# Kernel tuning notes

Measured on AMD Instinct MI355X. Metric: run time of the kernel, lower is better.

The kernel has to match this reference:

```python
import jax, jax.numpy as jnp
import numpy as np

N_NODES = 50000
N_EDGES = 600000
N_LABEL = 200000
IN_CH = 128
OUT_CH = 128
K_HOPS = 2


def setup_inputs() -> dict:
    key = jax.random.key(0)
    ks = jax.random.split(key, 9)
    x = jax.random.normal(ks[0], (N_NODES, IN_CH), dtype=jnp.float32)
    edge_index = jax.random.randint(ks[1], (2, N_EDGES), 0, N_NODES)
    edge_label_index = jax.random.randint(ks[2], (2, N_LABEL), 0, N_NODES)
    conv_weight = jax.random.normal(ks[3], (OUT_CH, IN_CH), dtype=jnp.float32) * 0.05
    conv_bias = jax.random.normal(ks[4], (OUT_CH,), dtype=jnp.float32) * 0.05
    w1 = jax.random.normal(ks[5], (OUT_CH // 2, OUT_CH), dtype=jnp.float32) * 0.05
    b1 = jax.random.normal(ks[6], (OUT_CH // 2,), dtype=jnp.float32) * 0.05
    w2 = jax.random.normal(ks[7], (1, OUT_CH // 2), dtype=jnp.float32) * 0.05
    b2 = jax.random.normal(ks[8], (1,), dtype=jnp.float32) * 0.05
    return {"x": x, "edge_index": edge_index, "edge_label_index": edge_label_index,
            "conv_weight": conv_weight, "conv_bias": conv_bias,
            "w1": w1, "b1": b1, "w2": w2, "b2": b2}


def reference(x, edge_index, edge_label_index, conv_weight, conv_bias, w1, b1, w2, b2):
    n = x.shape[0]
    # gcn_norm with self-loops: A_hat = D^{-1/2} (A + I) D^{-1/2}
    loop = jnp.arange(n, dtype=edge_index.dtype)
    src = jnp.concatenate([edge_index[0], loop])  # message sources
    dst = jnp.concatenate([edge_index[1], loop])  # aggregation targets
    deg = jax.ops.segment_sum(jnp.ones_like(dst, dtype=x.dtype), dst, num_segments=n)
    dinv = jnp.where(deg > 0, jax.lax.rsqrt(deg), 0.0)
    w = dinv[src] * dinv[dst]  # [E+N] edge weights

    # K-hop propagation: h <- A_hat h, repeated K times (SGConv)
    h = x
    for _ in range(K_HOPS):
        h = jax.ops.segment_sum(h[src] * w[:, None], dst, num_segments=n)
    z = h @ conv_weight.T + conv_bias  # [N, out_channels]

    # decode: gather endpoint embeddings, multiply, tiny MLP (dropout inactive at eval)
    s = z[edge_label_index[0]] * z[edge_label_index[1]]  # [E_label, out]
    h1 = jax.nn.relu(s @ w1.T + b1)
    r = (h1 @ w2.T + b2).sum(axis=-1)  # [E_label]
    return r
```

## Files before the change

### kernel.cpp

```cpp
#include <hip/hip_runtime.h>

#define N_CH 128

typedef _Float16 half8  __attribute__((ext_vector_type(8)));
typedef _Float16 half4v __attribute__((ext_vector_type(4)));
typedef float    floatx4 __attribute__((ext_vector_type(4)));


__global__ void k_zero(int* __restrict__ cnt, int n) {
    int i = blockIdx.x * blockDim.x + threadIdx.x;
    if (i < n) cnt[i] = 0;
}

__global__ void k_count(const int* __restrict__ dst, int* __restrict__ cnt, int E) {
    int e = blockIdx.x * blockDim.x + threadIdx.x;
    if (e < E) atomicAdd(&cnt[dst[e]], 1);
}

__global__ __launch_bounds__(1024) void k_scan1(const int* __restrict__ cnt,
                                                int* __restrict__ offs,
                                                int* __restrict__ bsum, int n) {
    __shared__ int ssum[16];
    int tid = threadIdx.x;
    int lane = tid & 63, wid = tid >> 6;
    int i = blockIdx.x * 1024 + tid;
    int v = (i < n) ? cnt[i] : 0;
    int x = v;
    #pragma unroll
    for (int off = 1; off < 64; off <<= 1) {
        int y = __shfl_up(x, off, 64);
        if (lane >= off) x += y;
    }
    if (lane == 63) ssum[wid] = x;
    __syncthreads();
    if (wid == 0 && lane < 16) {
        int s = ssum[lane];
        #pragma unroll
        for (int off = 1; off < 16; off <<= 1) {
            int y = __shfl_up(s, off, 64);
            if (lane >= off) s += y;
        }
        ssum[lane] = s;
    }
    __syncthreads();
    int waveoff = (wid > 0) ? ssum[wid - 1] : 0;
    int incl = x + waveoff;
    if (i < n) offs[i] = incl - v;
    if (tid == 1023) bsum[blockIdx.x] = incl;
}

__global__ __launch_bounds__(64) void k_scan2(const int* __restrict__ bsum,
                                              int* __restrict__ bbase, int nb) {
    int lane = threadIdx.x;
    int v = (lane < nb) ? bsum[lane] : 0;
    int x = v;
    #pragma unroll
    for (int off = 1; off < 64; off <<= 1) {
        int y = __shfl_up(x, off, 64);
        if (lane >= off) x += y;
    }
    if (lane < nb) bbase[lane] = x - v;
}

__global__ void k_scan3(const int* __restrict__ cnt, int* __restrict__ offs,
                        const int* __restrict__ bbase, int* __restrict__ cur,
                        float* __restrict__ dinv, int n) {
    int i = blockIdx.x * blockDim.x + threadIdx.x;
    if (i < n) {
        int o = offs[i] + bbase[i >> 10];
        offs[i] = o;
        cur[i]  = o;
        dinv[i] = rsqrtf((float)(cnt[i] + 1));
    }
}

__global__ void k_fill(const int* __restrict__ src, const int* __restrict__ dst,
                       int* __restrict__ cur, int* __restrict__ csr, int E) {
    int e = blockIdx.x * blockDim.x + threadIdx.x;
    if (e < E) {
        int p = atomicAdd(&cur[dst[e]], 1);
        csr[p] = src[e];
    }
}


__global__ void k_cvt(const float* __restrict__ x, const float* __restrict__ dinv,
                      _Float16* __restrict__ u0, _Float16* __restrict__ u1,
                      const float* __restrict__ W,  _Float16* __restrict__ wh,
                      const float* __restrict__ W1, _Float16* __restrict__ w1h,
                      int n) {
    int nx4  = n * (N_CH / 4);
    int nw4  = N_CH * N_CH / 4;
    int nw14 = 64 * N_CH / 4;
    int i = blockIdx.x * blockDim.x + threadIdx.x;
    if (i < nx4) {
        float d = dinv[i >> 5];
        float4 v = ((const float4*)x)[i];
        half4v o;
        o[0] = (_Float16)(d * v.x); o[1] = (_Float16)(d * v.y);
        o[2] = (_Float16)(d * v.z); o[3] = (_Float16)(d * v.w);
        ((half4v*)u0)[i] = o;
        return;
    }
    int j = i - nx4;
    if (j < nw4) {
        float4 v = ((const float4*)W)[j];
        half4v o;
        o[0] = (_Float16)v.x; o[1] = (_Float16)v.y; o[2] = (_Float16)v.z; o[3] = (_Float16)v.w;
        ((half4v*)wh)[j] = o;
        return;
    }
    j -= nw4;
    if (j < nw14) {
        float4 v = ((const float4*)W1)[j];
        half4v o;
        o[0] = (_Float16)v.x; o[1] = (_Float16)v.y; o[2] = (_Float16)v.z; o[3] = (_Float16)v.w;
        ((half4v*)w1h)[j] = o;
        return;
    }
    j -= nw14;
    if (j < 64) {
        half4v zz; zz[0] = (_Float16)0.f; zz[1] = (_Float16)0.f; zz[2] = (_Float16)0.f; zz[3] = (_Float16)0.f;
        _Float16* dst16 = (j < 32) ? u0 : u1;
        ((half4v*)(dst16 + (size_t)n * N_CH))[j & 31] = zz;
    }
}


__global__ __launch_bounds__(256) void k_hop16(const _Float16* __restrict__ hin,
                                               _Float16* __restrict__ hout,
                                               const int* __restrict__ offs,
                                               const int* __restrict__ cnt,
                                               const float* __restrict__ dinv,
                                               const int* __restrict__ csr,
                                               int n, int squared) {
    int tid  = threadIdx.x;
    int node = blockIdx.x * 16 + (tid >> 4);
    int c16  = tid & 15;
    if (node >= n) return;
    float di = dinv[node];
    float sc = squared ? di * di : di;
    int s0 = offs[node], c = cnt[node];
    const int* lst = csr + s0;
    half8 self = ((const half8*)(hin + (size_t)node * N_CH))[c16];
    float acc[8];
    #pragma unroll
    for (int j = 0; j < 8; ++j) acc[j] = (float)self[j];
    for (int t0 = 0; t0 < c; t0 += 8) {
        int idx[8];
        #pragma unroll
        for (int i = 0; i < 8; ++i) {
            int t = t0 + i;
            int v = lst[t];
            idx[i] = (t < c) ? v : n;
        }
        half8 u[8];
        #pragma unroll
        for (int i = 0; i < 8; ++i)
            u[i] = ((const half8*)(hin + (size_t)idx[i] * N_CH))[c16];
        #pragma unroll
        for (int i = 0; i < 8; ++i)
            #pragma unroll
            for (int j = 0; j < 8; ++j) acc[j] += (float)u[i][j];
    }
    half8 o;
    #pragma unroll
    for (int j = 0; j < 8; ++j) o[j] = (_Float16)(sc * acc[j]);
    ((half8*)(hout + (size_t)node * N_CH))[c16] = o;
}


__global__ __launch_bounds__(256) void k_zlin_mfma(const _Float16* __restrict__ h,
                                                   const _Float16* __restrict__ wh,
                                                   const float* __restrict__ bc,
                                                   _Float16* __restrict__ z, int n) {
    __shared__ half8 wls[128 * 16];
    int tid = threadIdx.x;
    int lane = tid & 63, w = tid >> 6;
    int quad = lane >> 4, m16 = lane & 15;
    int nb = blockIdx.x * 64;
    #pragma unroll
    for (int i = 0; i < 8; ++i) {
        int g = tid + 256 * i;
        int r = g >> 4, c = g & 15;
        wls[r * 16 + (c ^ (r & 15))] = ((const half8*)wh)[g];
    }
    int arow = nb + w * 16 + m16;
    const half8* hrow = (const half8*)(h + (size_t)arow * N_CH);
    half8 a[4];
    #pragma unroll
    for (int kk = 0; kk < 4; ++kk) a[kk] = hrow[kk * 4 + quad];
    __syncthreads();
    int outnode0 = nb + w * 16 + quad * 4;
    #pragma unroll
    for (int jt = 0; jt < 8; ++jt) {
        floatx4 acc = {0.f, 0.f, 0.f, 0.f};
        #pragma unroll
        for (int kk = 0; kk < 4; ++kk) {
            int r = jt * 16 + m16;
            half8 bfr = wls[r * 16 + ((kk * 4 + quad) ^ m16)];
            acc = __builtin_amdgcn_mfma_f32_16x16x32_f16(a[kk], bfr, acc, 0, 0, 0);
        }
        int j = jt * 16 + m16;
        float bias = bc[j];
        #pragma unroll
        for (int reg = 0; reg < 4; ++reg) {
            int node = outnode0 + reg;
            if (node < n) z[(size_t)node * N_CH + j] = (_Float16)(acc[reg] + bias);
        }
    }
}


__global__ __launch_bounds__(256) void k_decode_mfma(const _Float16* __restrict__ z,
        const int* __restrict__ ai, const int* __restrict__ bi,
        const _Float16* __restrict__ w1h, const float* __restrict__ b1,
        const float* __restrict__ w2, const float* __restrict__ b2,
        float* __restrict__ out, int m) {
    __shared__ half8 w1ls[64 * 16];
    __shared__ half8 sls[64 * 16];
    int tid = threadIdx.x;
    int lane = tid & 63, w = tid >> 6;
    int quad = lane >> 4, m16 = lane & 15;
    int pbase = blockIdx.x * 64;
    #pragma unroll
    for (int i = 0; i < 4; ++i) {
        int g = tid + 256 * i;
        int r = g >> 4, c = g & 15;
        w1ls[r * 16 + (c ^ (r & 15))] = ((const half8*)w1h)[g];
    }
    int pidx = pbase + w * 16 + m16;
    if (pidx >= m) pidx = m - 1;
    int idxa = ai[pidx];
    int idxb = bi[pidx];
    #pragma unroll
    for (int it = 0; it < 4; ++it) {
        int p = it * 4 + quad;
        int ia = __shfl(idxa, p, 64);
        int ib = __shfl(idxb, p, 64);
        half8 za = ((const half8*)(z + (size_t)ia * N_CH))[m16];
        half8 zb = ((const half8*)(z + (size_t)ib * N_CH))[m16];
        half8 s8 = za * zb;
        int pp = w * 16 + p;
        sls[pp * 16 + (m16 ^ (pp & 15))] = s8;
    }
    __syncthreads();
    half8 a[4];
    #pragma unroll
    for (int kk = 0; kk < 4; ++kk)
        a[kk] = sls[(w * 16 + m16) * 16 + ((kk * 4 + quad) ^ m16)];
    float rsum[4] = {0.f, 0.f, 0.f, 0.f};
    #pragma unroll
    for (int jt = 0; jt < 4; ++jt) {
        floatx4 acc = {0.f, 0.f, 0.f, 0.f};
        #pragma unroll
        for (int kk = 0; kk < 4; ++kk) {
            int r = jt * 16 + m16;
            half8 bfr = w1ls[r * 16 + ((kk * 4 + quad) ^ m16)];
            acc = __builtin_amdgcn_mfma_f32_16x16x32_f16(a[kk], bfr, acc, 0, 0, 0);
        }
        int j = jt * 16 + m16;
        float b1j = b1[j], w2j = w2[j];
        #pragma unroll
        for (int reg = 0; reg < 4; ++reg) {
            float v = fmaxf(acc[reg] + b1j, 0.f) * w2j;
            v += __shfl_xor(v, 1, 64);
            v += __shfl_xor(v, 2, 64);
            v += __shfl_xor(v, 4, 64);
            v += __shfl_xor(v, 8, 64);
            rsum[reg] += v;
        }
    }
    if (m16 == 0) {
        float bb = b2[0];
        #pragma unroll
        for (int reg = 0; reg < 4; ++reg) {
            int gp = pbase + w * 16 + quad * 4 + reg;
            if (gp < m) out[gp] = rsum[reg] + bb;
        }
    }
}


extern "C" void kernel_launch(void* const* d_in, const int* in_sizes, int n_in,
                              void* d_out, int out_size, void* d_ws, size_t ws_size,
                              hipStream_t stream) {
    const float* x   = (const float*)d_in[0];
    const int*   ei  = (const int*)d_in[1];
    const int*   eli = (const int*)d_in[2];
    const float* W   = (const float*)d_in[3];
    const float* bc  = (const float*)d_in[4];
    const float* W1  = (const float*)d_in[5];
    const float* b1  = (const float*)d_in[6];
    const float* w2  = (const float*)d_in[7];
    const float* b2  = (const float*)d_in[8];
    float* out = (float*)d_out;

    const int N = in_sizes[0] / N_CH;
    const int E = in_sizes[1] / 2;
    const int M = in_sizes[2] / 2;

    const int* src = ei;
    const int* dst = ei + E;
    const int* ai  = eli;
    const int* bi  = eli + M;

    _Float16* hb0 = (_Float16*)d_ws;
    _Float16* hb1 = hb0 + (size_t)(N + 1) * N_CH;
    _Float16* wh  = hb1 + (size_t)(N + 1) * N_CH;
    _Float16* w1h = wh + 16384;
    int*   csr  = (int*)(w1h + 8192);
    int*   cnt  = csr + E;
    int*   off  = cnt + N;
    int*   cur  = off + N;
    float* dnv  = (float*)(cur + N);
    int*   bsum = (int*)(dnv + N);
    int*   bbas = bsum + 64;

    int nb = (N + 1023) / 1024;
    k_zero<<<(N + 255) / 256, 256, 0, stream>>>(cnt, N);
    k_count<<<(E + 255) / 256, 256, 0, stream>>>(dst, cnt, E);
    k_scan1<<<nb, 1024, 0, stream>>>(cnt, off, bsum, N);
    k_scan2<<<1, 64, 0, stream>>>(bsum, bbas, nb);
    k_scan3<<<(N + 255) / 256, 256, 0, stream>>>(cnt, off, bbas, cur, dnv, N);
    k_fill<<<(E + 255) / 256, 256, 0, stream>>>(src, dst, cur, csr, E);
    int tot4 = N * (N_CH / 4) + N_CH * N_CH / 4 + 64 * N_CH / 4 + 64;
    k_cvt<<<(tot4 + 255) / 256, 256, 0, stream>>>(x, dnv, hb0, hb1, W, wh, W1, w1h, N);

    int hop_blocks = (N + 15) / 16;
    k_hop16<<<hop_blocks, 256, 0, stream>>>(hb0, hb1, off, cnt, dnv, csr, N, 1);
    k_hop16<<<hop_blocks, 256, 0, stream>>>(hb1, hb0, off, cnt, dnv, csr, N, 0);

    k_zlin_mfma<<<(N + 63) / 64, 256, 0, stream>>>(hb0, wh, bc, hb1, N);

    k_decode_mfma<<<(M + 63) / 64, 256, 0, stream>>>(hb1, ai, bi, w1h, b1, w2, b2, out, M);
}
```

Measured before the change: 233.7 us.

## Widen hop gather batch, use fdot2 accumulation, batch decode loads, memset counts

The hop kernel now gathers 16 neighbor rows per batch instead of 8, which puts more independent loads in flight. It accumulates each half pair into fp32 with fdot2 instead of separate converts and adds. The decode kernel issues all endpoint gathers before multiplying, so the loads can overlap. The zeroing kernel is replaced by hipMemsetAsync. The cost is higher register pressure in the hop kernel and wasted padded loads for low-degree nodes, which is most of them at an average degree of about 12.

Result: slower. 239.1 us (+2.3%).

```diff
diff --git a/kernel.cpp b/kernel.cpp
--- a/kernel.cpp
+++ b/kernel.cpp
@@ -4,13 +4,9 @@
 
 typedef _Float16 half8  __attribute__((ext_vector_type(8)));
 typedef _Float16 half4v __attribute__((ext_vector_type(4)));
+typedef _Float16 half2v __attribute__((ext_vector_type(2)));
 typedef float    floatx4 __attribute__((ext_vector_type(4)));
 
-
-__global__ void k_zero(int* __restrict__ cnt, int n) {
-    int i = blockIdx.x * blockDim.x + threadIdx.x;
-    if (i < n) cnt[i] = 0;
-}
 
 __global__ void k_count(const int* __restrict__ dst, int* __restrict__ cnt, int E) {
     int e = blockIdx.x * blockDim.x + threadIdx.x;
@@ -143,25 +139,34 @@
     int s0 = offs[node], c = cnt[node];
     const int* lst = csr + s0;
     half8 self = ((const half8*)(hin + (size_t)node * N_CH))[c16];
+    const half2v c10 = {(_Float16)1.0f, (_Float16)0.0f};
+    const half2v c01 = {(_Float16)0.0f, (_Float16)1.0f};
     float acc[8];
     #pragma unroll
     for (int j = 0; j < 8; ++j) acc[j] = (float)self[j];
-    for (int t0 = 0; t0 < c; t0 += 8) {
-        int idx[8];
-        #pragma unroll
-        for (int i = 0; i < 8; ++i) {
+    for (int t0 = 0; t0 < c; t0 += 16) {
+        int idx[16];
+        #pragma unroll
+        for (int i = 0; i < 16; ++i) {
             int t = t0 + i;
             int v = lst[t];
             idx[i] = (t < c) ? v : n;
         }
-        half8 u[8];
-        #pragma unroll
-        for (int i = 0; i < 8; ++i)
+        half8 u[16];
+        #pragma unroll
+        for (int i = 0; i < 16; ++i)
             u[i] = ((const half8*)(hin + (size_t)idx[i] * N_CH))[c16];
         #pragma unroll
-        for (int i = 0; i < 8; ++i)
+        for (int i = 0; i < 16; ++i) {
             #pragma unroll
-            for (int j = 0; j < 8; ++j) acc[j] += (float)u[i][j];
+            for (int p = 0; p < 4; ++p) {
+                half2v pair;
+                pair[0] = u[i][2 * p];
+                pair[1] = u[i][2 * p + 1];
+                acc[2 * p]     = __builtin_amdgcn_fdot2(pair, c10, acc[2 * p], false);
+                acc[2 * p + 1] = __builtin_amdgcn_fdot2(pair, c01, acc[2 * p + 1], false);
+            }
+        }
     }
     half8 o;
     #pragma unroll
@@ -233,15 +238,23 @@
     if (pidx >= m) pidx = m - 1;
     int idxa = ai[pidx];
     int idxb = bi[pidx];
+    int ia[4], ib[4];
     #pragma unroll
     for (int it = 0; it < 4; ++it) {
         int p = it * 4 + quad;
-        int ia = __shfl(idxa, p, 64);
-        int ib = __shfl(idxb, p, 64);
-        half8 za = ((const half8*)(z + (size_t)ia * N_CH))[m16];
-        half8 zb = ((const half8*)(z + (size_t)ib * N_CH))[m16];
-        half8 s8 = za * zb;
-        int pp = w * 16 + p;
+        ia[it] = __shfl(idxa, p, 64);
+        ib[it] = __shfl(idxb, p, 64);
+    }
+    half8 za[4], zb[4];
+    #pragma unroll
+    for (int it = 0; it < 4; ++it) {
+        za[it] = ((const half8*)(z + (size_t)ia[it] * N_CH))[m16];
+        zb[it] = ((const half8*)(z + (size_t)ib[it] * N_CH))[m16];
+    }
+    #pragma unroll
+    for (int it = 0; it < 4; ++it) {
+        half8 s8 = za[it] * zb[it];
+        int pp = w * 16 + it * 4 + quad;
         sls[pp * 16 + (m16 ^ (pp & 15))] = s8;
     }
     __syncthreads();
@@ -318,7 +331,7 @@
     int*   bbas = bsum + 64;
 
     int nb = (N + 1023) / 1024;
-    k_zero<<<(N + 255) / 256, 256, 0, stream>>>(cnt, N);
+    (void)hipMemsetAsync(cnt, 0, (size_t)N * sizeof(int), stream);
     k_count<<<(E + 255) / 256, 256, 0, stream>>>(dst, cnt, E);
     k_scan1<<<nb, 1024, 0, stream>>>(cnt, off, bsum, N);
     k_scan2<<<1, 64, 0, stream>>>(bsum, bbas, nb);
```

## Merge setup kernels, single-block scan, 16-bit CSR indices, batched decode gathers

Applied to the files above, without the earlier changes.

Folds the zeroing kernel and the weight conversion into one prep kernel and replaces the three-kernel scan with a single-block looping scan, which cuts kernel launches. CSR neighbor indices are stored as 16-bit unsigned values to halve index traffic in the hop kernels. The decode kernel now issues all endpoint gathers before using any of them, to raise memory-level parallelism. The single-block scan serialises about 50 iterations on one CU. The 16-bit indices only cover node ids below 65536, which holds for this input size.

Measured after the change: 278.2 us. 1.19x slower.

```diff
diff --git a/kernel.cpp b/kernel.cpp
--- a/kernel.cpp
+++ b/kernel.cpp
@@ -7,92 +7,94 @@
 typedef float    floatx4 __attribute__((ext_vector_type(4)));
 
 
-__global__ void k_zero(int* __restrict__ cnt, int n) {
+__global__ void k_prep(const float* __restrict__ x, const float* __restrict__ dinv_unused,
+                       int* __restrict__ cnt,
+                       const float* __restrict__ W,  _Float16* __restrict__ wh,
+                       const float* __restrict__ W1, _Float16* __restrict__ w1h,
+                       int n) {
     int i = blockIdx.x * blockDim.x + threadIdx.x;
     if (i < n) cnt[i] = 0;
-}
+    int nw4  = N_CH * N_CH / 4;
+    int nw14 = 64 * N_CH / 4;
+    if (i < nw4) {
+        float4 v = ((const float4*)W)[i];
+        half4v o;
+        o[0] = (_Float16)v.x; o[1] = (_Float16)v.y; o[2] = (_Float16)v.z; o[3] = (_Float16)v.w;
+        ((half4v*)wh)[i] = o;
+    } else if (i < nw4 + nw14) {
+        int j = i - nw4;
+        float4 v = ((const float4*)W1)[j];
+        half4v o;
+        o[0] = (_Float16)v.x; o[1] = (_Float16)v.y; o[2] = (_Float16)v.z; o[3] = (_Float16)v.w;
+        ((half4v*)w1h)[j] = o;
+    }
+}
+
 
 __global__ void k_count(const int* __restrict__ dst, int* __restrict__ cnt, int E) {
     int e = blockIdx.x * blockDim.x + threadIdx.x;
     if (e < E) atomicAdd(&cnt[dst[e]], 1);
 }
 
-__global__ __launch_bounds__(1024) void k_scan1(const int* __restrict__ cnt,
-                                                int* __restrict__ offs,
-                                                int* __restrict__ bsum, int n) {
+__global__ __launch_bounds__(1024) void k_scan(const int* __restrict__ cnt,
+                                               int* __restrict__ offs,
+                                               int* __restrict__ cur,
+                                               float* __restrict__ dinv, int n) {
     __shared__ int ssum[16];
+    __shared__ int sbase;
     int tid = threadIdx.x;
     int lane = tid & 63, wid = tid >> 6;
-    int i = blockIdx.x * 1024 + tid;
-    int v = (i < n) ? cnt[i] : 0;
-    int x = v;
-    #pragma unroll
-    for (int off = 1; off < 64; off <<= 1) {
-        int y = __shfl_up(x, off, 64);
-        if (lane >= off) x += y;
-    }
-    if (lane == 63) ssum[wid] = x;
+    if (tid == 0) sbase = 0;
     __syncthreads();
-    if (wid == 0 && lane < 16) {
-        int s = ssum[lane];
-        #pragma unroll
-        for (int off = 1; off < 16; off <<= 1) {
-            int y = __shfl_up(s, off, 64);
-            if (lane >= off) s += y;
-        }
-        ssum[lane] = s;
-    }
-    __syncthreads();
-    int waveoff = (wid > 0) ? ssum[wid - 1] : 0;
-    int incl = x + waveoff;
-    if (i < n) offs[i] = incl - v;
-    if (tid == 1023) bsum[blockIdx.x] = incl;
-}
-
-__global__ __launch_bounds__(64) void k_scan2(const int* __restrict__ bsum,
-                                              int* __restrict__ bbase, int nb) {
-    int lane = threadIdx.x;
-    int v = (lane < nb) ? bsum[lane] : 0;
-    int x = v;
-    #pragma unroll
-    for (int off = 1; off < 64; off <<= 1) {
-        int y = __shfl_up(x, off, 64);
-        if (lane >= off) x += y;
-    }
-    if (lane < nb) bbase[lane] = x - v;
-}
-
-__global__ void k_scan3(const int* __restrict__ cnt, int* __restrict__ offs,
-                        const int* __restrict__ bbase, int* __restrict__ cur,
-                        float* __restrict__ dinv, int n) {
-    int i = blockIdx.x * blockDim.x + threadIdx.x;
-    if (i < n) {
-        int o = offs[i] + bbase[i >> 10];
-        offs[i] = o;
-        cur[i]  = o;
-        dinv[i] = rsqrtf((float)(cnt[i] + 1));
+    for (int base = 0; base < n; base += 1024) {
+        int i = base + tid;
+        int v = (i < n) ? cnt[i] : 0;
+        int x = v;
+        #pragma unroll
+        for (int off = 1; off < 64; off <<= 1) {
+            int y = __shfl_up(x, off, 64);
+            if (lane >= off) x += y;
+        }
+        if (lane == 63) ssum[wid] = x;
+        __syncthreads();
+        if (wid == 0 && lane < 16) {
+            int s = ssum[lane];
+            #pragma unroll
+            for (int off = 1; off < 16; off <<= 1) {
+                int y = __shfl_up(s, off, 64);
+                if (lane >= off) s += y;
+            }
+            ssum[lane] = s;
+        }
+        __syncthreads();
+        int waveoff = (wid > 0) ? ssum[wid - 1] : 0;
+        int incl = x + waveoff + sbase;
+        if (i < n) {
+            int excl = incl - v;
+            offs[i] = excl;
+            cur[i]  = excl;
+            dinv[i] = rsqrtf((float)(v + 1));
+        }
+        __syncthreads();
+        if (tid == 1023) sbase = incl;
+        __syncthreads();
     }
 }
 
 __global__ void k_fill(const int* __restrict__ src, const int* __restrict__ dst,
-                       int* __restrict__ cur, int* __restrict__ csr, int E) {
+                       int* __restrict__ cur, unsigned short* __restrict__ csr, int E) {
     int e = blockIdx.x * blockDim.x + threadIdx.x;
     if (e < E) {
         int p = atomicAdd(&cur[dst[e]], 1);
-        csr[p] = src[e];
-    }
-}
-
-
-__global__ void k_cvt(const float* __restrict__ x, const float* __restrict__ dinv,
-                      _Float16* __restrict__ u0, _Float16* __restrict__ u1,
-                      const float* __restrict__ W,  _Float16* __restrict__ wh,
-                      const float* __restrict__ W1, _Float16* __restrict__ w1h,
-                      int n) {
-    int nx4  = n * (N_CH / 4);
-    int nw4  = N_CH * N_CH / 4;
-    int nw14 = 64 * N_CH / 4;
+        csr[p] = (unsigned short)src[e];
+    }
+}
+
+
+__global__ void k_scale(const float* __restrict__ x, const float* __restrict__ dinv,
+                        _Float16* __restrict__ u0, _Float16* __restrict__ u1, int n) {
     int i = blockIdx.x * blockDim.x + threadIdx.x;
+    int nx4 = n * (N_CH / 4);
     if (i < nx4) {
         float d = dinv[i >> 5];
         float4 v = ((const float4*)x)[i];
@@ -100,26 +102,8 @@
         o[0] = (_Float16)(d * v.x); o[1] = (_Float16)(d * v.y);
         o[2] = (_Float16)(d * v.z); o[3] = (_Float16)(d * v.w);
         ((half4v*)u0)[i] = o;
-        return;
-    }
-    int j = i - nx4;
-    if (j < nw4) {
-        float4 v = ((const float4*)W)[j];
-        half4v o;
-        o[0] = (_Float16)v.x; o[1] = (_Float16)v.y; o[2] = (_Float16)v.z; o[3] = (_Float16)v.w;
-        ((half4v*)wh)[j] = o;
-        return;
-    }
-    j -= nw4;
-    if (j < nw14) {
-        float4 v = ((const float4*)W1)[j];
-        half4v o;
-        o[0] = (_Float16)v.x; o[1] = (_Float16)v.y; o[2] = (_Float16)v.z; o[3] = (_Float16)v.w;
-        ((half4v*)w1h)[j] = o;
-        return;
-    }
-    j -= nw14;
-    if (j < 64) {
+    } else if (i < nx4 + 64) {
+        int j = i - nx4;
         half4v zz; zz[0] = (_Float16)0.f; zz[1] = (_Float16)0.f; zz[2] = (_Float16)0.f; zz[3] = (_Float16)0.f;
         _Float16* dst16 = (j < 32) ? u0 : u1;
         ((half4v*)(dst16 + (size_t)n * N_CH))[j & 31] = zz;
@@ -132,7 +116,7 @@
                                                const int* __restrict__ offs,
                                                const int* __restrict__ cnt,
                                                const float* __restrict__ dinv,
-                                               const int* __restrict__ csr,
+                                               const unsigned short* __restrict__ csr,
                                                int n, int squared) {
     int tid  = threadIdx.x;
     int node = blockIdx.x * 16 + (tid >> 4);
@@ -141,7 +125,7 @@
     float di = dinv[node];
     float sc = squared ? di * di : di;
     int s0 = offs[node], c = cnt[node];
-    const int* lst = csr + s0;
+    const unsigned short* lst = csr + s0;
     half8 self = ((const half8*)(hin + (size_t)node * N_CH))[c16];
     float acc[8];
     #pragma unroll
@@ -151,8 +135,8 @@
         #pragma unroll
         for (int i = 0; i < 8; ++i) {
             int t = t0 + i;
-            int v = lst[t];
-            idx[i] = (t < c) ? v : n;
+            unsigned short v = lst[t];
+            idx[i] = (t < c) ? (int)v : n;
         }
         half8 u[8];
         #pragma unroll
@@ -233,15 +217,23 @@
     if (pidx >= m) pidx = m - 1;
     int idxa = ai[pidx];
     int idxb = bi[pidx];
+    int ia[4], ib[4];
     #pragma unroll
     for (int it = 0; it < 4; ++it) {
         int p = it * 4 + quad;
-        int ia = __shfl(idxa, p, 64);
-        int ib = __shfl(idxb, p, 64);
-        half8 za = ((const half8*)(z + (size_t)ia * N_CH))[m16];
-        half8 zb = ((const half8*)(z + (size_t)ib * N_CH))[m16];
-        half8 s8 = za * zb;
-        int pp = w * 16 + p;
+        ia[it] = __shfl(idxa, p, 64);
+        ib[it] = __shfl(idxb, p, 64);
+    }
+    half8 za[4], zb[4];
+    #pragma unroll
+    for (int it = 0; it < 4; ++it) {
+        za[it] = ((const half8*)(z + (size_t)ia[it] * N_CH))[m16];
+        zb[it] = ((const half8*)(z + (size_t)ib[it] * N_CH))[m16];
+    }
+    #pragma unroll
+    for (int it = 0; it < 4; ++it) {
+        half8 s8 = za[it] * zb[it];
+        int pp = w * 16 + it * 4 + quad;
         sls[pp * 16 + (m16 ^ (pp & 15))] = s8;
     }
     __syncthreads();
@@ -309,23 +301,19 @@
     _Float16* hb1 = hb0 + (size_t)(N + 1) * N_CH;
     _Float16* wh  = hb1 + (size_t)(N + 1) * N_CH;
     _Float16* w1h = wh + 16384;
-    int*   csr  = (int*)(w1h + 8192);
-    int*   cnt  = csr + E;
+    unsigned short* csr = (unsigned short*)(w1h + 8192);
+    int*   cnt  = (int*)(csr + E);
     int*   off  = cnt + N;
     int*   cur  = off + N;
     float* dnv  = (float*)(cur + N);
-    int*   bsum = (int*)(dnv + N);
-    int*   bbas = bsum + 64;
-
-    int nb = (N + 1023) / 1024;
-    k_zero<<<(N + 255) / 256, 256, 0, stream>>>(cnt, N);
+
+    int prep_work = N;
+    k_prep<<<(prep_work + 255) / 256, 256, 0, stream>>>(x, dnv, cnt, W, wh, W1, w1h, N);
     k_count<<<(E + 255) / 256, 256, 0, stream>>>(dst, cnt, E);
-    k_scan1<<<nb, 1024, 0, stream>>>(cnt, off, bsum, N);
-    k_scan2<<<1, 64, 0, stream>>>(bsum, bbas, nb);
-    k_scan3<<<(N + 255) / 256, 256, 0, stream>>>(cnt, off, bbas, cur, dnv, N);
+    k_scan<<<1, 1024, 0, stream>>>(cnt, off, cur, dnv, N);
     k_fill<<<(E + 255) / 256, 256, 0, stream>>>(src, dst, cur, csr, E);
-    int tot4 = N * (N_CH / 4) + N_CH * N_CH / 4 + 64 * N_CH / 4 + 64;
-    k_cvt<<<(tot4 + 255) / 256, 256, 0, stream>>>(x, dnv, hb0, hb1, W, wh, W1, w1h, N);
+    int sc_work = N * (N_CH / 4) + 64;
+    k_scale<<<(sc_work + 255) / 256, 256, 0, stream>>>(x, dnv, hb0, hb1, N);
 
     int hop_blocks = (N + 15) / 16;
     k_hop16<<<hop_blocks, 256, 0, stream>>>(hb0, hb1, off, cnt, dnv, csr, N, 1);
```
